# Kernel tuning notes

Measured on AMD Instinct MI355X. Metric: run time of the kernel, lower is better.

## Reference

```python
import jax, jax.numpy as jnp
import numpy as np

D_MODEL = 1024
D_INNER = 2048   # expand * d_model
D_STATE = 16
D_CONV = 4
DT_RANK = 64     # d_model // 16
EPS = 1e-5


def setup_inputs() -> dict:
    key = jax.random.key(0)
    ks = jax.random.split(key, 8)
    s = 0.02
    A_log = jnp.log(jnp.broadcast_to(
        jnp.arange(1, D_STATE + 1, dtype=jnp.float32), (D_INNER, D_STATE)))
    return {
        "hidden_states": jax.random.normal(ks[0], (2, 1024, D_MODEL), jnp.float32),
        "norm_w": jnp.ones((D_MODEL,), jnp.float32),
        "in_proj_w": jax.random.normal(ks[1], (2 * D_INNER, D_MODEL), jnp.float32) * s,
        "conv_w": jax.random.normal(ks[2], (D_INNER, 1, D_CONV), jnp.float32) * s,
        "conv_b": jnp.zeros((D_INNER,), jnp.float32),
        "x_proj_w": jax.random.normal(ks[3], (DT_RANK + 2 * D_STATE, D_INNER), jnp.float32) * s,
        "dt_proj_w": jax.random.normal(ks[4], (D_INNER, DT_RANK), jnp.float32) * s,
        "dt_proj_b": jax.random.normal(ks[5], (D_INNER,), jnp.float32) * 0.1,
        "A_log": A_log,
        "D": jnp.ones((D_INNER,), jnp.float32),
        "out_proj_w": jax.random.normal(ks[6], (D_MODEL, D_INNER), jnp.float32) * s,
    }


def _mamba_block(hidden_states, norm_w, in_proj_w, conv_w, conv_b,
                 x_proj_w, dt_proj_w, dt_proj_b, A_log, D, out_proj_w):
    residual = hidden_states
    # pre RMSNorm
    x = hidden_states
    x = x * jax.lax.rsqrt(jnp.mean(x * x, axis=-1, keepdims=True) + EPS) * norm_w
    # input projection -> (x, z) gate split, each (B, L, d_inner)
    xz = jnp.einsum('bld,ed->ble', x, in_proj_w)
    xin, z = jnp.split(xz, 2, axis=-1)
    # causal depthwise conv1d over time
    xc = jax.lax.conv_general_dilated(
        xin.transpose(0, 2, 1), conv_w, window_strides=(1,),
        padding=[(D_CONV - 1, 0)], dimension_numbers=('NCH', 'OIH', 'NCH'),
        feature_group_count=D_INNER)
    xin = jax.nn.silu(xc.transpose(0, 2, 1) + conv_b)
    # data-dependent SSM params
    dbl = jnp.einsum('bld,ed->ble', xin, x_proj_w)
    dt, Bm, Cm = jnp.split(dbl, [DT_RANK, DT_RANK + D_STATE], axis=-1)
    delta = jax.nn.softplus(jnp.einsum('blr,dr->bld', dt, dt_proj_w) + dt_proj_b)
    A = -jnp.exp(A_log)  # (d_inner, d_state)

    def step(h, inp):
        d_t, B_t, C_t, x_t = inp  # (B,d_inner), (B,N), (B,N), (B,d_inner)
        h = jnp.exp(d_t[..., None] * A) * h + (d_t * x_t)[..., None] * B_t[:, None, :]
        y_t = jnp.einsum('bdn,bn->bd', h, C_t)
        return h, y_t

    Bsz = hidden_states.shape[0]
    h0 = jnp.zeros((Bsz, D_INNER, D_STATE), hidden_states.dtype)
    _, ys = jax.lax.scan(step, h0, (delta.transpose(1, 0, 2), Bm.transpose(1, 0, 2),
                                    Cm.transpose(1, 0, 2), xin.transpose(1, 0, 2)))
    y = ys.transpose(1, 0, 2) + xin * D  # skip term
    y = y * jax.nn.silu(z)               # gate
    out = jnp.einsum('bld,ed->ble', y, out_proj_w)
    return out + residual


def reference(hidden_states, norm_w, in_proj_w, conv_w, conv_b,
              x_proj_w, dt_proj_w, dt_proj_b, A_log, D, out_proj_w):
    return _mamba_block(hidden_states, norm_w, in_proj_w, conv_w, conv_b,
                        x_proj_w, dt_proj_w, dt_proj_b, A_log, D, out_proj_w)
```

## Files before the change

### kernel.cpp

```cpp
#include <hip/hip_runtime.h>
#include <math.h>

#define D_MODEL 1024
#define D_INNER 2048
#define D_STATE 16
#define DT_RANK 64
#define NROWS   2048
#define XZ_LD   4096
#define DBL_LD  96
#define EPS     1e-5f
#define NCH     32
#define CLEN    32
#define DGRP    128

typedef __attribute__((ext_vector_type(8))) short short8;
typedef __attribute__((ext_vector_type(4))) float v4f;

__device__ __forceinline__ float sigmoidf_(float x) { return 1.f / (1.f + __expf(-x)); }
__device__ __forceinline__ float softplusf_(float x) {
    return fmaxf(x, 0.f) + log1pf(__expf(-fabsf(x)));
}
__device__ __forceinline__ unsigned short f2bf(float f) {
    union { float f; unsigned u; } v; v.f = f;
    unsigned r = v.u + 0x7fff + ((v.u >> 16) & 1);
    return (unsigned short)(r >> 16);
}
__device__ __forceinline__ float bf2f(unsigned short u) {
    return __uint_as_float(((unsigned)u) << 16);
}
__device__ __forceinline__ void glds16(const void* g, void* l) {
    __builtin_amdgcn_global_load_lds(
        (const __attribute__((address_space(1))) unsigned*)g,
        (__attribute__((address_space(3))) unsigned*)l, 16, 0, 0);
}

__global__ __launch_bounds__(256)
void rmsnorm_kernel(const float* __restrict__ x, const float* __restrict__ w,
                    unsigned short* __restrict__ out)
{
    const int row = blockIdx.x;
    const int t = threadIdx.x;
    const float4 xv = ((const float4*)(x + (size_t)row * D_MODEL))[t];
    float s = xv.x*xv.x + xv.y*xv.y + xv.z*xv.z + xv.w*xv.w;
    #pragma unroll
    for (int off = 32; off > 0; off >>= 1) s += __shfl_down(s, off, 64);
    __shared__ float red[4];
    if ((t & 63) == 0) red[t >> 6] = s;
    __syncthreads();
    s = red[0] + red[1] + red[2] + red[3];
    const float rs = rsqrtf(s * (1.f / D_MODEL) + EPS);
    const float4 wv = ((const float4*)w)[t];
    ushort4 o;
    o.x = f2bf(xv.x * rs * wv.x); o.y = f2bf(xv.y * rs * wv.y);
    o.z = f2bf(xv.z * rs * wv.z); o.w = f2bf(xv.w * rs * wv.w);
    ((ushort4*)(out + (size_t)row * D_MODEL))[t] = o;
}

__global__ __launch_bounds__(256)
void f2bf3_kernel(const float* __restrict__ win, const float* __restrict__ wout,
                  const float* __restrict__ wx,
                  unsigned short* __restrict__ win_bf, unsigned short* __restrict__ wout_bf,
                  unsigned short* __restrict__ wx_bf)
{
    int i = blockIdx.x * 256 + threadIdx.x;
    const float* src; unsigned short* dst; int valid4;
    if (i < 1048576) {
        src = win; dst = win_bf; valid4 = 1048576;
    } else if ((i -= 1048576) < 524288) {
        src = wout; dst = wout_bf; valid4 = 524288;
    } else if ((i -= 524288) < 65536) {
        src = wx; dst = wx_bf; valid4 = 49152;
    } else return;
    ushort4 o;
    if (i < valid4) {
        const float4 v = ((const float4*)src)[i];
        o.x = f2bf(v.x); o.y = f2bf(v.y); o.z = f2bf(v.z); o.w = f2bf(v.w);
    } else { o.x = 0; o.y = 0; o.z = 0; o.w = 0; }
    ((ushort4*)dst)[i] = o;
}

template<bool RES, bool NGUARD>
__global__ __launch_bounds__(256)
void gemm_mfma(const unsigned short* __restrict__ A, int lda,
               const unsigned short* __restrict__ B, int ldb,
               float* __restrict__ C, int ldc, size_t czStride,
               const float* __restrict__ res, int ldr,
               int N, int kLen)
{
    __shared__ unsigned short As[4096];
    __shared__ unsigned short Bs[4096];
    const int tid  = threadIdx.x;
    const int lane = tid & 63;
    const int wave = tid >> 6;
    const int m0 = blockIdx.y * 128;
    const int n0 = blockIdx.x * 128;
    const int kOff = blockIdx.z * kLen;
    C += (size_t)blockIdx.z * czStride;

    const int sr = wave * 32 + (lane >> 2);
    const int sc = (lane & 3) * 8;
    const unsigned short* gA = A + (size_t)(m0 + sr) * lda + kOff + sc;
    const unsigned short* gB = B + (size_t)(n0 + sr) * ldb + kOff + sc;
    unsigned short* lA = As + wave * 1024 + lane * 8;
    unsigned short* lB = Bs + wave * 1024 + lane * 8;

    const int wm = (wave & 1) * 64;
    const int wn = (wave >> 1) * 64;
    const int ar = wm + (lane & 15);
    const int br = wn + (lane & 15);
    const int fk = (lane >> 4) * 8;

    v4f acc[4][4] = {};

    for (int k0 = 0; k0 < kLen; k0 += 32) {
        __syncthreads();
        glds16(gA + k0,            lA);
        glds16(gA + k0 + 16*lda,   lA + 512);
        glds16(gB + k0,            lB);
        glds16(gB + k0 + 16*ldb,   lB + 512);
        __syncthreads();
        short8 af[4], bfv[4];
        #pragma unroll
        for (int mi = 0; mi < 4; mi++)
            af[mi] = *(const short8*)&As[(ar + mi*16) * 32 + fk];
        #pragma unroll
        for (int ni = 0; ni < 4; ni++)
            bfv[ni] = *(const short8*)&Bs[(br + ni*16) * 32 + fk];
        #pragma unroll
        for (int mi = 0; mi < 4; mi++)
            #pragma unroll
            for (int ni = 0; ni < 4; ni++)
                acc[mi][ni] = __builtin_amdgcn_mfma_f32_16x16x32_bf16(
                    af[mi], bfv[ni], acc[mi][ni], 0, 0, 0);
    }

    const int er = (lane >> 4) * 4;
    const int ec = lane & 15;
    #pragma unroll
    for (int mi = 0; mi < 4; mi++) {
        #pragma unroll
        for (int r = 0; r < 4; r++) {
            const int row = m0 + wm + mi*16 + er + r;
            #pragma unroll
            for (int ni = 0; ni < 4; ni++) {
                const int col = n0 + wn + ni*16 + ec;
                if (!NGUARD || col < N) {
                    float v = acc[mi][ni][r];
                    if (RES) v += res[(size_t)row * ldr + col];
                    C[(size_t)row * ldc + col] = v;
                }
            }
        }
    }
}

__global__ __launch_bounds__(256)
void reduce8_kernel(const float* __restrict__ part, float* __restrict__ dbl)
{
    const int i = blockIdx.x * 256 + threadIdx.x;
    float4 s = ((const float4*)part)[i];
    #pragma unroll
    for (int z = 1; z < 8; z++) {
        const float4 p = ((const float4*)(part + (size_t)z * 196608))[i];
        s.x += p.x; s.y += p.y; s.z += p.z; s.w += p.w;
    }
    ((float4*)dbl)[i] = s;
}

__global__ __launch_bounds__(256)
void reduce4res_kernel(const float* __restrict__ part, const float* __restrict__ hs,
                       float* __restrict__ out)
{
    const int i = blockIdx.x * 256 + threadIdx.x;
    float4 s = ((const float4*)hs)[i];
    #pragma unroll
    for (int z = 0; z < 4; z++) {
        const float4 p = ((const float4*)(part + (size_t)z * NROWS * D_MODEL))[i];
        s.x += p.x; s.y += p.y; s.z += p.z; s.w += p.w;
    }
    ((float4*)out)[i] = s;
}

template<int ACT, bool BIAS>
__global__ __launch_bounds__(256)
void gemm_nt(const float* __restrict__ A, int lda,
             const float* __restrict__ B, int ldb,
             float* __restrict__ C, int ldc,
             const float* __restrict__ bias,
             int N, int K)
{
    __shared__ float As[16][68];
    __shared__ float Bs[16][68];
    const int tid = threadIdx.x;
    const int m0 = blockIdx.y * 64;
    const int n0 = blockIdx.x * 64;
    const int r  = tid >> 2;
    const int c4 = (tid & 3) << 2;
    const int tx = tid & 15;
    const int ty = tid >> 4;
    const bool bok = (n0 + r) < N;
    float acc[4][4] = {};

    for (int k0 = 0; k0 < K; k0 += 16) {
        const float4 av = *(const float4*)(A + (size_t)(m0 + r) * lda + k0 + c4);
        float4 bv = make_float4(0.f, 0.f, 0.f, 0.f);
        if (bok) bv = *(const float4*)(B + (size_t)(n0 + r) * ldb + k0 + c4);
        __syncthreads();
        As[c4+0][r] = av.x; As[c4+1][r] = av.y; As[c4+2][r] = av.z; As[c4+3][r] = av.w;
        Bs[c4+0][r] = bv.x; Bs[c4+1][r] = bv.y; Bs[c4+2][r] = bv.z; Bs[c4+3][r] = bv.w;
        __syncthreads();
        #pragma unroll
        for (int k = 0; k < 16; k++) {
            const float4 a = *(const float4*)&As[k][ty << 2];
            const float4 b = *(const float4*)&Bs[k][tx << 2];
            const float aa[4] = {a.x, a.y, a.z, a.w};
            const float bb[4] = {b.x, b.y, b.z, b.w};
            #pragma unroll
            for (int i = 0; i < 4; i++)
                #pragma unroll
                for (int j = 0; j < 4; j++)
                    acc[i][j] = fmaf(aa[i], bb[j], acc[i][j]);
        }
    }
    #pragma unroll
    for (int i = 0; i < 4; i++) {
        const int m = m0 + (ty << 2) + i;
        #pragma unroll
        for (int j = 0; j < 4; j++) {
            const int n = n0 + (tx << 2) + j;
            if (n < N) {
                float v = acc[i][j];
                if (BIAS) v += bias[n];
                if (ACT == 1) v = softplusf_(v);
                C[(size_t)m * ldc + n] = v;
            }
        }
    }
}

__global__ __launch_bounds__(256)
void conv_silu_kernel(const float* __restrict__ xz, const float* __restrict__ cw,
                      const float* __restrict__ cb, unsigned short* __restrict__ xin_bf)
{
    const int idx = blockIdx.x * 256 + threadIdx.x;
    const int d   = idx & (D_INNER - 1);
    const int row = idx >> 11;
    const int b   = row >> 10;
    const int l   = row & 1023;
    float acc = cb[d];
    #pragma unroll
    for (int j = 0; j < 4; j++) {
        const int ll = l + j - 3;
        if (ll >= 0)
            acc = fmaf(cw[d * 4 + j], xz[(size_t)(b * 1024 + ll) * XZ_LD + d], acc);
    }
    xin_bf[(size_t)row * D_INNER + d] = f2bf(acc * sigmoidf_(acc));
}


__global__ __launch_bounds__(128)
void scan_p1(const float* __restrict__ xz, const unsigned short* __restrict__ xin_bf,
             const float* __restrict__ dbl_, const float* __restrict__ alog,
             float* __restrict__ Ssum, unsigned short* __restrict__ Hend)
{
    __shared__ float  sdl[CLEN][DGRP];
    __shared__ unsigned short sxi[CLEN][DGRP];
    __shared__ float  sB[CLEN][16];
    const int tid = threadIdx.x;
    const int d0  = blockIdx.x * DGRP;
    const int c   = blockIdx.y;
    const int b   = blockIdx.z;
    const int d   = d0 + tid;
    const int lbase = b * 1024 + c * CLEN;

    float Av[16];
    #pragma unroll
    for (int n = 0; n < 16; n++) Av[n] = -__expf(alog[d * D_STATE + n]);

    #pragma unroll
    for (int i = 0; i < 8; i++) {
        const int idx = i * DGRP + tid;
        const int l = idx >> 5;
        const int c4 = (idx & 31) << 2;
        *(float4*)&sdl[l][c4]  = *(const float4*)&xz[(size_t)(lbase + l) * XZ_LD + d0 + c4];
        *(ushort4*)&sxi[l][c4] = *(const ushort4*)&xin_bf[(size_t)(lbase + l) * D_INNER + d0 + c4];
    }
    for (int t = tid; t < CLEN * 16; t += DGRP) {
        const int l = t >> 4, n = t & 15;
        sB[l][n] = dbl_[(size_t)(lbase + l) * DBL_LD + DT_RANK + n];
    }
    __syncthreads();

    float h[16] = {};
    float S = 0.f;
    for (int l = 0; l < CLEN; l++) {
        const float dv = sdl[l][tid];
        const float dx = dv * bf2f(sxi[l][tid]);
        S += dv;
        const float4 B0 = *(const float4*)&sB[l][0];
        const float4 B1 = *(const float4*)&sB[l][4];
        const float4 B2 = *(const float4*)&sB[l][8];
        const float4 B3 = *(const float4*)&sB[l][12];
        const float Bv[16] = {B0.x,B0.y,B0.z,B0.w, B1.x,B1.y,B1.z,B1.w,
                              B2.x,B2.y,B2.z,B2.w, B3.x,B3.y,B3.z,B3.w};
        #pragma unroll
        for (int n = 0; n < 16; n++) {
            const float a = __expf(dv * Av[n]);
            h[n] = fmaf(a, h[n], dx * Bv[n]);
        }
    }
    const size_t od = (size_t)(b * NCH + c) * D_INNER + d;
    Ssum[od] = S;
    ushort4* Hp = (ushort4*)&Hend[od * D_STATE];
    #pragma unroll
    for (int q = 0; q < 4; q++) {
        ushort4 o;
        o.x = f2bf(h[q*4+0]); o.y = f2bf(h[q*4+1]);
        o.z = f2bf(h[q*4+2]); o.w = f2bf(h[q*4+3]);
        Hp[q] = o;
    }
}

__global__ __launch_bounds__(256)
void scan_p2(const float* __restrict__ alog, const float* __restrict__ Ssum,
             unsigned short* __restrict__ Hend)
{
    const int i = blockIdx.x * 256 + threadIdx.x;
    const int n = i & 15;
    const int d = (i >> 4) & (D_INNER - 1);
    const int b = i >> 15;
    const float Av = -__expf(alog[d * D_STATE + n]);
    float h = 0.f;
    for (int c = 0; c < NCH; c++) {
        const size_t od = (size_t)(b * NCH + c) * D_INNER + d;
        const float P  = __expf(Av * Ssum[od]);
        const size_t o = od * D_STATE + n;
        const float he = bf2f(Hend[o]);
        Hend[o] = f2bf(h);
        h = fmaf(P, h, he);
    }
}

__global__ __launch_bounds__(128)
void scan_p3(const float* __restrict__ xz, const unsigned short* __restrict__ xin_bf,
             const float* __restrict__ dbl_, const float* __restrict__ alog,
             const float* __restrict__ Dvec, const unsigned short* __restrict__ Hstart,
             unsigned short* __restrict__ y_bf)
{
    __shared__ float  sdl[CLEN][DGRP];
    __shared__ float  sz [CLEN][DGRP];
    __shared__ unsigned short sxi[CLEN][DGRP];
    __shared__ float  sB[CLEN][16];
    __shared__ float  sC[CLEN][16];
    const int tid = threadIdx.x;
    const int d0  = blockIdx.x * DGRP;
    const int c   = blockIdx.y;
    const int b   = blockIdx.z;
    const int d   = d0 + tid;
    const int lbase = b * 1024 + c * CLEN;

    float Av[16];
    #pragma unroll
    for (int n = 0; n < 16; n++) Av[n] = -__expf(alog[d * D_STATE + n]);
    const float Dd = Dvec[d];

    #pragma unroll
    for (int i = 0; i < 8; i++) {
        const int idx = i * DGRP + tid;
        const int l = idx >> 5;
        const int c4 = (idx & 31) << 2;
        *(float4*)&sdl[l][c4]  = *(const float4*)&xz[(size_t)(lbase + l) * XZ_LD + d0 + c4];
        *(float4*)&sz [l][c4]  = *(const float4*)&xz[(size_t)(lbase + l) * XZ_LD + D_INNER + d0 + c4];
        *(ushort4*)&sxi[l][c4] = *(const ushort4*)&xin_bf[(size_t)(lbase + l) * D_INNER + d0 + c4];
    }
    for (int t = tid; t < CLEN * 16; t += DGRP) {
        const int l = t >> 4, n = t & 15;
        sB[l][n] = dbl_[(size_t)(lbase + l) * DBL_LD + DT_RANK + n];
        sC[l][n] = dbl_[(size_t)(lbase + l) * DBL_LD + DT_RANK + D_STATE + n];
    }

    float h[16];
    {
        const ushort4* Hp = (const ushort4*)&Hstart[((size_t)(b * NCH + c) * D_INNER + d) * D_STATE];
        #pragma unroll
        for (int q = 0; q < 4; q++) {
            const ushort4 v = Hp[q];
            h[q*4+0] = bf2f(v.x); h[q*4+1] = bf2f(v.y);
            h[q*4+2] = bf2f(v.z); h[q*4+3] = bf2f(v.w);
        }
    }
    __syncthreads();

    for (int l = 0; l < CLEN; l++) {
        const float dv = sdl[l][tid];
        const float xv = bf2f(sxi[l][tid]);
        const float dx = dv * xv;
        const float4 B0 = *(const float4*)&sB[l][0];
        const float4 B1 = *(const float4*)&sB[l][4];
        const float4 B2 = *(const float4*)&sB[l][8];
        const float4 B3 = *(const float4*)&sB[l][12];
        const float4 C0 = *(const float4*)&sC[l][0];
        const float4 C1 = *(const float4*)&sC[l][4];
        const float4 C2 = *(const float4*)&sC[l][8];
        const float4 C3 = *(const float4*)&sC[l][12];
        const float Bv[16] = {B0.x,B0.y,B0.z,B0.w, B1.x,B1.y,B1.z,B1.w,
                              B2.x,B2.y,B2.z,B2.w, B3.x,B3.y,B3.z,B3.w};
        const float Cv[16] = {C0.x,C0.y,C0.z,C0.w, C1.x,C1.y,C1.z,C1.w,
                              C2.x,C2.y,C2.z,C2.w, C3.x,C3.y,C3.z,C3.w};
        float y0 = 0.f, y1 = 0.f, y2 = 0.f, y3 = 0.f;
        #pragma unroll
        for (int n = 0; n < 16; n += 4) {
            float a;
            a = __expf(dv * Av[n+0]); h[n+0] = fmaf(a, h[n+0], dx * Bv[n+0]); y0 = fmaf(h[n+0], Cv[n+0], y0);
            a = __expf(dv * Av[n+1]); h[n+1] = fmaf(a, h[n+1], dx * Bv[n+1]); y1 = fmaf(h[n+1], Cv[n+1], y1);
            a = __expf(dv * Av[n+2]); h[n+2] = fmaf(a, h[n+2], dx * Bv[n+2]); y2 = fmaf(h[n+2], Cv[n+2], y2);
            a = __expf(dv * Av[n+3]); h[n+3] = fmaf(a, h[n+3], dx * Bv[n+3]); y3 = fmaf(h[n+3], Cv[n+3], y3);
        }
        const float y = ((y0 + y1) + (y2 + y3)) + xv * Dd;
        const float z = sz[l][tid];
        y_bf[(size_t)(lbase + l) * D_INNER + d] = f2bf(y * z * sigmoidf_(z));
    }
}

extern "C" void kernel_launch(void* const* d_in, const int* in_sizes, int n_in,
                              void* d_out, int out_size, void* d_ws, size_t ws_size,
                              hipStream_t stream)
{
    const float* hs   = (const float*)d_in[0];
    const float* norw = (const float*)d_in[1];
    const float* win  = (const float*)d_in[2];
    const float* cw   = (const float*)d_in[3];
    const float* cb   = (const float*)d_in[4];
    const float* wx   = (const float*)d_in[5];
    const float* wdt  = (const float*)d_in[6];
    const float* bdt  = (const float*)d_in[7];
    const float* alog = (const float*)d_in[8];
    const float* Dv   = (const float*)d_in[9];
    const float* wout = (const float*)d_in[10];
    float* out = (float*)d_out;

    float* ws = (float*)d_ws;
    float*          xz      = ws;
    float*          oppart  = xz;
    float*          dbl     = xz + (size_t)NROWS * XZ_LD;
    unsigned short* xn_bf   = (unsigned short*)(dbl + NROWS * DBL_LD);
    unsigned short* Hend    = xn_bf;
    unsigned short* xin_bf  = xn_bf + (size_t)NROWS * D_MODEL;
    unsigned short* shared_ = xin_bf + (size_t)NROWS * D_INNER;
    unsigned short* win_bf  = shared_;
    float*          part    = (float*)shared_;
    float*          Ssum    = (float*)shared_;
    unsigned short* y_bf    = shared_;
    unsigned short* wx_bf   = shared_ + (size_t)4096 * 1024;
    unsigned short* wout_bf = wx_bf + (size_t)128 * 2048;

    rmsnorm_kernel<<<NROWS, 256, 0, stream>>>(hs, norw, xn_bf);
    f2bf3_kernel<<<6400, 256, 0, stream>>>(win, wout, wx, win_bf, wout_bf, wx_bf);
    gemm_mfma<false,false><<<dim3(32, 16, 1), 256, 0, stream>>>(
        xn_bf, D_MODEL, win_bf, D_MODEL, xz, XZ_LD, 0, nullptr, 0, 4096, D_MODEL);
    conv_silu_kernel<<<(NROWS * D_INNER) / 256, 256, 0, stream>>>(xz, cw, cb, xin_bf);
    gemm_mfma<false,true><<<dim3(1, 16, 8), 256, 0, stream>>>(
        xin_bf, D_INNER, wx_bf, D_INNER, part, DBL_LD, (size_t)NROWS * DBL_LD,
        nullptr, 0, DBL_LD, D_INNER / 8);
    reduce8_kernel<<<192, 256, 0, stream>>>(part, dbl);
    gemm_nt<1,true><<<dim3(32, 32), 256, 0, stream>>>(
        dbl, DBL_LD, wdt, DT_RANK, xz, XZ_LD, bdt, D_INNER, DT_RANK);
    scan_p1<<<dim3(D_INNER / DGRP, NCH, 2), DGRP, 0, stream>>>(xz, xin_bf, dbl, alog, Ssum, Hend);
    scan_p2<<<256, 256, 0, stream>>>(alog, Ssum, Hend);
    scan_p3<<<dim3(D_INNER / DGRP, NCH, 2), DGRP, 0, stream>>>(xz, xin_bf, dbl, alog, Dv, Hend, y_bf);
    gemm_mfma<false,false><<<dim3(8, 16, 4), 256, 0, stream>>>(
        y_bf, D_INNER, wout_bf, D_INNER, oppart, D_MODEL, (size_t)NROWS * D_MODEL,
        nullptr, 0, 1024, D_INNER / 4);
    reduce4res_kernel<<<2048, 256, 0, stream>>>(oppart, hs, out);
}
```

Measured before the change: 277.9 us.

## Merge prep kernels, move dt_proj to bf16 MFMA GEMM, deepen GEMM K-step

```diff
diff --git a/kernel.cpp b/kernel.cpp
--- a/kernel.cpp
+++ b/kernel.cpp
@@ -35,34 +35,34 @@
 }
 
 __global__ __launch_bounds__(256)
-void rmsnorm_kernel(const float* __restrict__ x, const float* __restrict__ w,
-                    unsigned short* __restrict__ out)
-{
-    const int row = blockIdx.x;
+void prep_kernel(const float* __restrict__ hs, const float* __restrict__ norw,
+                 const float* __restrict__ win, const float* __restrict__ wout,
+                 const float* __restrict__ wx, const float* __restrict__ wdt,
+                 unsigned short* __restrict__ xn_bf, unsigned short* __restrict__ win_bf,
+                 unsigned short* __restrict__ wout_bf, unsigned short* __restrict__ wx_bf,
+                 unsigned short* __restrict__ wdt_bf)
+{
+    const int bid = blockIdx.x;
     const int t = threadIdx.x;
-    const float4 xv = ((const float4*)(x + (size_t)row * D_MODEL))[t];
-    float s = xv.x*xv.x + xv.y*xv.y + xv.z*xv.z + xv.w*xv.w;
-    #pragma unroll
-    for (int off = 32; off > 0; off >>= 1) s += __shfl_down(s, off, 64);
-    __shared__ float red[4];
-    if ((t & 63) == 0) red[t >> 6] = s;
-    __syncthreads();
-    s = red[0] + red[1] + red[2] + red[3];
-    const float rs = rsqrtf(s * (1.f / D_MODEL) + EPS);
-    const float4 wv = ((const float4*)w)[t];
-    ushort4 o;
-    o.x = f2bf(xv.x * rs * wv.x); o.y = f2bf(xv.y * rs * wv.y);
-    o.z = f2bf(xv.z * rs * wv.z); o.w = f2bf(xv.w * rs * wv.w);
-    ((ushort4*)(out + (size_t)row * D_MODEL))[t] = o;
-}
-
-__global__ __launch_bounds__(256)
-void f2bf3_kernel(const float* __restrict__ win, const float* __restrict__ wout,
-                  const float* __restrict__ wx,
-                  unsigned short* __restrict__ win_bf, unsigned short* __restrict__ wout_bf,
-                  unsigned short* __restrict__ wx_bf)
-{
-    int i = blockIdx.x * 256 + threadIdx.x;
+    if (bid < 2048) {
+        const int row = bid;
+        const float4 xv = ((const float4*)(hs + (size_t)row * D_MODEL))[t];
+        float s = xv.x*xv.x + xv.y*xv.y + xv.z*xv.z + xv.w*xv.w;
+        #pragma unroll
+        for (int off = 32; off > 0; off >>= 1) s += __shfl_down(s, off, 64);
+        __shared__ float red[4];
+        if ((t & 63) == 0) red[t >> 6] = s;
+        __syncthreads();
+        s = red[0] + red[1] + red[2] + red[3];
+        const float rs = rsqrtf(s * (1.f / D_MODEL) + EPS);
+        const float4 wv = ((const float4*)norw)[t];
+        ushort4 o;
+        o.x = f2bf(xv.x * rs * wv.x); o.y = f2bf(xv.y * rs * wv.y);
+        o.z = f2bf(xv.z * rs * wv.z); o.w = f2bf(xv.w * rs * wv.w);
+        ((ushort4*)(xn_bf + (size_t)row * D_MODEL))[t] = o;
+        return;
+    }
+    int i = (bid - 2048) * 256 + t;
     const float* src; unsigned short* dst; int valid4;
     if (i < 1048576) {
         src = win; dst = win_bf; valid4 = 1048576;
@@ -70,6 +70,8 @@
         src = wout; dst = wout_bf; valid4 = 524288;
     } else if ((i -= 524288) < 65536) {
         src = wx; dst = wx_bf; valid4 = 49152;
+    } else if ((i -= 65536) < 32768) {
+        src = wdt; dst = wdt_bf; valid4 = 32768;
     } else return;
     ushort4 o;
     if (i < valid4) {
@@ -79,16 +81,19 @@
     ((ushort4*)dst)[i] = o;
 }
 
-template<bool RES, bool NGUARD>
+template<int ACT, bool BIAS, bool RES, bool NGUARD>
 __global__ __launch_bounds__(256)
 void gemm_mfma(const unsigned short* __restrict__ A, int lda,
                const unsigned short* __restrict__ B, int ldb,
                float* __restrict__ C, int ldc, size_t czStride,
+               const float* __restrict__ bias,
                const float* __restrict__ res, int ldr,
                int N, int kLen)
 {
-    __shared__ unsigned short As[4096];
-    __shared__ unsigned short Bs[4096];
+    __shared__ unsigned short As0[4096];
+    __shared__ unsigned short As1[4096];
+    __shared__ unsigned short Bs0[4096];
+    __shared__ unsigned short Bs1[4096];
     const int tid  = threadIdx.x;
     const int lane = tid & 63;
     const int wave = tid >> 6;
@@ -101,8 +106,7 @@
     const int sc = (lane & 3) * 8;
     const unsigned short* gA = A + (size_t)(m0 + sr) * lda + kOff + sc;
     const unsigned short* gB = B + (size_t)(n0 + sr) * ldb + kOff + sc;
-    unsigned short* lA = As + wave * 1024 + lane * 8;
-    unsigned short* lB = Bs + wave * 1024 + lane * 8;
+    const int lo = wave * 1024 + lane * 8;
 
     const int wm = (wave & 1) * 64;
     const int wn = (wave >> 1) * 64;
@@ -112,26 +116,35 @@
 
     v4f acc[4][4] = {};
 
-    for (int k0 = 0; k0 < kLen; k0 += 32) {
+    for (int k0 = 0; k0 < kLen; k0 += 64) {
         __syncthreads();
-        glds16(gA + k0,            lA);
-        glds16(gA + k0 + 16*lda,   lA + 512);
-        glds16(gB + k0,            lB);
-        glds16(gB + k0 + 16*ldb,   lB + 512);
+        glds16(gA + k0,                 As0 + lo);
+        glds16(gA + k0 + 16*lda,        As0 + lo + 512);
+        glds16(gA + k0 + 32,            As1 + lo);
+        glds16(gA + k0 + 32 + 16*lda,   As1 + lo + 512);
+        glds16(gB + k0,                 Bs0 + lo);
+        glds16(gB + k0 + 16*ldb,        Bs0 + lo + 512);
+        glds16(gB + k0 + 32,            Bs1 + lo);
+        glds16(gB + k0 + 32 + 16*ldb,   Bs1 + lo + 512);
         __syncthreads();
-        short8 af[4], bfv[4];
-        #pragma unroll
-        for (int mi = 0; mi < 4; mi++)
-            af[mi] = *(const short8*)&As[(ar + mi*16) * 32 + fk];
-        #pragma unroll
-        for (int ni = 0; ni < 4; ni++)
-            bfv[ni] = *(const short8*)&Bs[(br + ni*16) * 32 + fk];
-        #pragma unroll
-        for (int mi = 0; mi < 4; mi++)
+        #pragma unroll
+        for (int hh = 0; hh < 2; hh++) {
+            const unsigned short* Ah = hh ? As1 : As0;
+            const unsigned short* Bh = hh ? Bs1 : Bs0;
+            short8 af[4], bfv[4];
+            #pragma unroll
+            for (int mi = 0; mi < 4; mi++)
+                af[mi] = *(const short8*)&Ah[(ar + mi*16) * 32 + fk];
             #pragma unroll
             for (int ni = 0; ni < 4; ni++)
-                acc[mi][ni] = __builtin_amdgcn_mfma_f32_16x16x32_bf16(
-                    af[mi], bfv[ni], acc[mi][ni], 0, 0, 0);
+                bfv[ni] = *(const short8*)&Bh[(br + ni*16) * 32 + fk];
+            #pragma unroll
+            for (int mi = 0; mi < 4; mi++)
+                #pragma unroll
+                for (int ni = 0; ni < 4; ni++)
+                    acc[mi][ni] = __builtin_amdgcn_mfma_f32_16x16x32_bf16(
+                        af[mi], bfv[ni], acc[mi][ni], 0, 0, 0);
+        }
     }
 
     const int er = (lane >> 4) * 4;
@@ -146,6 +159,8 @@
                 const int col = n0 + wn + ni*16 + ec;
                 if (!NGUARD || col < N) {
                     float v = acc[mi][ni][r];
+                    if (BIAS) v += bias[col];
+                    if (ACT == 1) v = softplusf_(v);
                     if (RES) v += res[(size_t)row * ldr + col];
                     C[(size_t)row * ldc + col] = v;
                 }
@@ -155,7 +170,8 @@
 }
 
 __global__ __launch_bounds__(256)
-void reduce8_kernel(const float* __restrict__ part, float* __restrict__ dbl)
+void reduce8dt_kernel(const float* __restrict__ part, float* __restrict__ dbl,
+                      unsigned short* __restrict__ dt_bf)
 {
     const int i = blockIdx.x * 256 + threadIdx.x;
     float4 s = ((const float4*)part)[i];
@@ -165,6 +181,14 @@
         s.x += p.x; s.y += p.y; s.z += p.z; s.w += p.w;
     }
     ((float4*)dbl)[i] = s;
+    const int e   = i * 4;
+    const int row = e / 96;
+    const int col = e - row * 96;
+    if (col < DT_RANK) {
+        ushort4 o;
+        o.x = f2bf(s.x); o.y = f2bf(s.y); o.z = f2bf(s.z); o.w = f2bf(s.w);
+        *(ushort4*)&dt_bf[(size_t)row * DT_RANK + col] = o;
+    }
 }
 
 __global__ __launch_bounds__(256)
@@ -179,63 +203,6 @@
         s.x += p.x; s.y += p.y; s.z += p.z; s.w += p.w;
     }
     ((float4*)out)[i] = s;
-}
-
-template<int ACT, bool BIAS>
-__global__ __launch_bounds__(256)
-void gemm_nt(const float* __restrict__ A, int lda,
-             const float* __restrict__ B, int ldb,
-             float* __restrict__ C, int ldc,
-             const float* __restrict__ bias,
-             int N, int K)
-{
-    __shared__ float As[16][68];
-    __shared__ float Bs[16][68];
-    const int tid = threadIdx.x;
-    const int m0 = blockIdx.y * 64;
-    const int n0 = blockIdx.x * 64;
-    const int r  = tid >> 2;
-    const int c4 = (tid & 3) << 2;
-    const int tx = tid & 15;
-    const int ty = tid >> 4;
-    const bool bok = (n0 + r) < N;
-    float acc[4][4] = {};
-
-    for (int k0 = 0; k0 < K; k0 += 16) {
-        const float4 av = *(const float4*)(A + (size_t)(m0 + r) * lda + k0 + c4);
-        float4 bv = make_float4(0.f, 0.f, 0.f, 0.f);
-        if (bok) bv = *(const float4*)(B + (size_t)(n0 + r) * ldb + k0 + c4);
-        __syncthreads();
-        As[c4+0][r] = av.x; As[c4+1][r] = av.y; As[c4+2][r] = av.z; As[c4+3][r] = av.w;
-        Bs[c4+0][r] = bv.x; Bs[c4+1][r] = bv.y; Bs[c4+2][r] = bv.z; Bs[c4+3][r] = bv.w;
-        __syncthreads();
-        #pragma unroll
-        for (int k = 0; k < 16; k++) {
-            const float4 a = *(const float4*)&As[k][ty << 2];
-            const float4 b = *(const float4*)&Bs[k][tx << 2];
-            const float aa[4] = {a.x, a.y, a.z, a.w};
-            const float bb[4] = {b.x, b.y, b.z, b.w};
-            #pragma unroll
-            for (int i = 0; i < 4; i++)
-                #pragma unroll
-                for (int j = 0; j < 4; j++)
-                    acc[i][j] = fmaf(aa[i], bb[j], acc[i][j]);
-        }
-    }
-    #pragma unroll
-    for (int i = 0; i < 4; i++) {
-        const int m = m0 + (ty << 2) + i;
-        #pragma unroll
-        for (int j = 0; j < 4; j++) {
-            const int n = n0 + (tx << 2) + j;
-            if (n < N) {
-                float v = acc[i][j];
-                if (BIAS) v += bias[n];
-                if (ACT == 1) v = softplusf_(v);
-                C[(size_t)m * ldc + n] = v;
-            }
-        }
-    }
 }
 
 __global__ __launch_bounds__(256)
@@ -453,23 +420,25 @@
     unsigned short* y_bf    = shared_;
     unsigned short* wx_bf   = shared_ + (size_t)4096 * 1024;
     unsigned short* wout_bf = wx_bf + (size_t)128 * 2048;
-
-    rmsnorm_kernel<<<NROWS, 256, 0, stream>>>(hs, norw, xn_bf);
-    f2bf3_kernel<<<6400, 256, 0, stream>>>(win, wout, wx, win_bf, wout_bf, wx_bf);
-    gemm_mfma<false,false><<<dim3(32, 16, 1), 256, 0, stream>>>(
-        xn_bf, D_MODEL, win_bf, D_MODEL, xz, XZ_LD, 0, nullptr, 0, 4096, D_MODEL);
+    unsigned short* dt_bf   = wout_bf + (size_t)1024 * 2048;
+    unsigned short* wdt_bf  = dt_bf + (size_t)NROWS * DT_RANK;
+
+    prep_kernel<<<8576, 256, 0, stream>>>(hs, norw, win, wout, wx, wdt,
+                                          xn_bf, win_bf, wout_bf, wx_bf, wdt_bf);
+    gemm_mfma<0,false,false,false><<<dim3(32, 16, 1), 256, 0, stream>>>(
+        xn_bf, D_MODEL, win_bf, D_MODEL, xz, XZ_LD, 0, nullptr, nullptr, 0, 4096, D_MODEL);
     conv_silu_kernel<<<(NROWS * D_INNER) / 256, 256, 0, stream>>>(xz, cw, cb, xin_bf);
-    gemm_mfma<false,true><<<dim3(1, 16, 8), 256, 0, stream>>>(
+    gemm_mfma<0,false,false,true><<<dim3(1, 16, 8), 256, 0, stream>>>(
         xin_bf, D_INNER, wx_bf, D_INNER, part, DBL_LD, (size_t)NROWS * DBL_LD,
-        nullptr, 0, DBL_LD, D_INNER / 8);
-    reduce8_kernel<<<192, 256, 0, stream>>>(part, dbl);
-    gemm_nt<1,true><<<dim3(32, 32), 256, 0, stream>>>(
-        dbl, DBL_LD, wdt, DT_RANK, xz, XZ_LD, bdt, D_INNER, DT_RANK);
+        nullptr, nullptr, 0, DBL_LD, D_INNER / 8);
+    reduce8dt_kernel<<<192, 256, 0, stream>>>(part, dbl, dt_bf);
+    gemm_mfma<1,true,false,false><<<dim3(16, 16, 1), 256, 0, stream>>>(
+        dt_bf, DT_RANK, wdt_bf, DT_RANK, xz, XZ_LD, 0, bdt, nullptr, 0, D_INNER, DT_RANK);
     scan_p1<<<dim3(D_INNER / DGRP, NCH, 2), DGRP, 0, stream>>>(xz, xin_bf, dbl, alog, Ssum, Hend);
     scan_p2<<<256, 256, 0, stream>>>(alog, Ssum, Hend);
     scan_p3<<<dim3(D_INNER / DGRP, NCH, 2), DGRP, 0, stream>>>(xz, xin_bf, dbl, alog, Dv, Hend, y_bf);
-    gemm_mfma<false,false><<<dim3(8, 16, 4), 256, 0, stream>>>(
+    gemm_mfma<0,false,false,false><<<dim3(8, 16, 4), 256, 0, stream>>>(
         y_bf, D_INNER, wout_bf, D_INNER, oppart, D_MODEL, (size_t)NROWS * D_MODEL,
-        nullptr, 0, 1024, D_INNER / 4);
+        nullptr, nullptr, 0, 1024, D_INNER / 4);
     reduce4res_kernel<<<2048, 256, 0, stream>>>(oppart, hs, out);
 }
```

After: 264.6 us. -4.8%, faster.
